# Kernel optimization log

Measured on AMD Instinct MI355X. Metric: run time of the kernel, lower is better.

Reference implementation:

```python
import jax, jax.numpy as jnp
import numpy as np
import math

EMBED_DIM = 1024
NUM_HEADS = 16
HEAD_DIM = EMBED_DIM // NUM_HEADS
SEGMENT_LENGTHS = [2048, 4096]
DILATION_RATES = [1, 2]
B, N = 1, 8192
IS_CAUSAL = True


def setup_inputs() -> dict:
    key = jax.random.key(0)
    ks = jax.random.split(key, 12)
    def w(k):
        return (jax.random.normal(k, (EMBED_DIM, EMBED_DIM), dtype=jnp.float32) * 0.02)
    inp = {
        'query': jax.random.normal(ks[0], (B, N, EMBED_DIM), dtype=jnp.float32),
        'key':   jax.random.normal(ks[1], (B, N, EMBED_DIM), dtype=jnp.float32),
        'value': jax.random.normal(ks[2], (B, N, EMBED_DIM), dtype=jnp.float32),
        'Wq': w(ks[3]), 'bq': jnp.zeros((EMBED_DIM,), jnp.float32),
        'Wk': w(ks[4]), 'bk': jnp.zeros((EMBED_DIM,), jnp.float32),
        'Wv': w(ks[5]), 'bv': jnp.zeros((EMBED_DIM,), jnp.float32),
        'Wo': w(ks[6]), 'bo': jnp.zeros((EMBED_DIM,), jnp.float32),
    }
    return inp


def _dilated_group_attention(q, k, v, seg_len, dilation, offset, causal):
    # q,k,v: [B, N, Hg, D] -> dilated block attention within segments
    b, n, hg, d = q.shape
    nseg = n // seg_len
    m = seg_len // dilation  # dilated subsequence length per segment
    idx = offset + dilation * jnp.arange(m)  # positions inside a segment
    def gather(x):
        return x.reshape(b, nseg, seg_len, hg, d)[:, :, idx]  # [B,nseg,m,Hg,D]
    qs, ks_, vs = gather(q), gather(k), gather(v)
    scale = 1.0 / math.sqrt(d)
    # [B,nseg,Hg,m,m]
    scores = jnp.einsum('bnihd,bnjhd->bnhij', qs, ks_) * scale
    if causal:
        mask = jnp.tril(jnp.ones((m, m), dtype=bool))
        scores = jnp.where(mask, scores, jnp.finfo(scores.dtype).min)
    attn = jax.nn.softmax(scores, axis=-1)
    out = jnp.einsum('bnhij,bnjhd->bnihd', attn, vs)  # [B,nseg,m,Hg,D]
    # scatter dilated outputs back to full segment positions (others zero)
    full = jnp.zeros((b, nseg, seg_len, hg, d), dtype=out.dtype)
    full = full.at[:, :, idx].set(out)
    return full.reshape(b, n, hg, d)


def reference(query, key, value, Wq, bq, Wk, bk, Wv, bv, Wo, bo):
    b, n, e = query.shape
    q = query @ Wq.T + bq
    k = key @ Wk.T + bk
    v = value @ Wv.T + bv
    q = q.reshape(b, n, NUM_HEADS, HEAD_DIM)
    k = k.reshape(b, n, NUM_HEADS, HEAD_DIM)
    v = v.reshape(b, n, NUM_HEADS, HEAD_DIM)
    num_groups = len(SEGMENT_LENGTHS)
    hpg = NUM_HEADS // num_groups  # heads per (segment, dilation) group
    outs = []
    for g in range(num_groups):
        s, r = SEGMENT_LENGTHS[g], DILATION_RATES[g]
        off = g % r
        hsl = slice(g * hpg, (g + 1) * hpg)
        outs.append(_dilated_group_attention(q[:, :, hsl], k[:, :, hsl], v[:, :, hsl],
                                             s, r, off, IS_CAUSAL))
    attn_out = jnp.concatenate(outs, axis=2).reshape(b, n, e)
    return attn_out @ Wo.T + bo
```

## Files before the change

kernel.cpp:

```cpp
#include <hip/hip_runtime.h>
#include <hip/hip_bf16.h>

typedef __attribute__((ext_vector_type(8))) __bf16 bf16x8;
typedef __attribute__((ext_vector_type(8))) unsigned short us8;
typedef __attribute__((ext_vector_type(4))) float f32x4;
typedef __attribute__((ext_vector_type(16))) float f32x16;
typedef __attribute__((ext_vector_type(2))) unsigned int uint2v;

#define N_TOK 8192
#define EMB 1024

static __device__ __forceinline__ unsigned short f2bf(float f) {
  union { __bf16 b; unsigned short u; } c;
  c.b = (__bf16)f;
  return c.u;
}

static __device__ __forceinline__ f32x4 mfma16(bf16x8 a, bf16x8 b, f32x4 c) {
  return __builtin_amdgcn_mfma_f32_16x16x32_bf16(a, b, c, 0, 0, 0);
}
static __device__ __forceinline__ f32x16 mfma32(bf16x8 a, bf16x8 b, f32x16 c) {
  return __builtin_amdgcn_mfma_f32_32x32x16_bf16(a, b, c, 0, 0, 0);
}
static __device__ __forceinline__ unsigned int cvtpk(float lo, float hi) {
  unsigned int r;
  asm("v_cvt_pk_bf16_f32 %0, %1, %2" : "=v"(r) : "v"(lo), "v"(hi));
  return r;
}
static __device__ __forceinline__ void gload16(const unsigned short* g, unsigned short* l) {
  __builtin_amdgcn_global_load_lds(
      (const __attribute__((address_space(1))) unsigned int*)g,
      (__attribute__((address_space(3))) unsigned int*)l, 16, 0, 0);
}

__global__ __launch_bounds__(256) void convall(
    const float* __restrict__ X0, const float* __restrict__ X1, const float* __restrict__ X2,
    const float* __restrict__ W0, const float* __restrict__ W1,
    const float* __restrict__ W2, const float* __restrict__ W3,
    unsigned short* __restrict__ Dq, unsigned short* __restrict__ Dk,
    unsigned short* __restrict__ Dv, unsigned short* __restrict__ Wb)
{
  const int bid = blockIdx.x;
  const float* src;
  unsigned short* dst;
  long base;
  if (bid < 6144) {
    const int t = bid >> 11;
    const int b = bid & 2047;
    src = (t == 0) ? X0 : (t == 1) ? X1 : X2;
    dst = (t == 0) ? Dq : (t == 1) ? Dk : Dv;
    base = ((long)b * 256 + threadIdx.x) * 16;
  } else {
    const int r = bid - 6144;
    const int t = r >> 8;
    const int b = r & 255;
    src = (t == 0) ? W0 : (t == 1) ? W1 : (t == 2) ? W2 : W3;
    dst = Wb + (size_t)t * EMB * EMB;
    base = ((long)b * 256 + threadIdx.x) * 16;
  }
  float4 f0 = *(const float4*)(src + base);
  float4 f1 = *(const float4*)(src + base + 4);
  float4 f2 = *(const float4*)(src + base + 8);
  float4 f3 = *(const float4*)(src + base + 12);
  us8 p0, p1;
  p0[0]=f2bf(f0.x); p0[1]=f2bf(f0.y); p0[2]=f2bf(f0.z); p0[3]=f2bf(f0.w);
  p0[4]=f2bf(f1.x); p0[5]=f2bf(f1.y); p0[6]=f2bf(f1.z); p0[7]=f2bf(f1.w);
  p1[0]=f2bf(f2.x); p1[1]=f2bf(f2.y); p1[2]=f2bf(f2.z); p1[3]=f2bf(f2.w);
  p1[4]=f2bf(f3.x); p1[5]=f2bf(f3.y); p1[6]=f2bf(f3.z); p1[7]=f2bf(f3.w);
  *(us8*)(dst + base)     = p0;
  *(us8*)(dst + base + 8) = p1;
}

__global__ __launch_bounds__(256) void qkv_gemm4(
    const unsigned short* __restrict__ Xq, const unsigned short* __restrict__ Xk,
    const unsigned short* __restrict__ Xv, const unsigned short* __restrict__ Wb,
    const float* __restrict__ bq, const float* __restrict__ bk, const float* __restrict__ bv,
    unsigned short* __restrict__ O0, unsigned short* __restrict__ O1, unsigned short* __restrict__ O2)
{
  __shared__ __align__(16) unsigned short As[128 * 32];
  __shared__ __align__(16) unsigned short Bs[128 * 32];

  const int z = blockIdx.z;
  const unsigned short* X = (z == 0) ? Xq : (z == 1) ? Xk : Xv;
  const unsigned short* W = Wb + (size_t)z * EMB * EMB;
  const float* bias = (z == 0) ? bq : (z == 1) ? bk : bv;

  const int lin  = blockIdx.x;
  const int work = (lin & 7) * 64 + (lin >> 3);
  const long brow = (long)(work >> 3) * 128;
  const long bcol = (long)(work & 7) * 128;

  const int tid  = threadIdx.x;
  const int lane = tid & 63;
  const int w    = tid >> 6;
  const int wrb  = (w >> 1) * 64;
  const int wcb  = (w & 1) * 64;
  const int r16  = lane & 15;
  const int kq   = (lane >> 4) * 8;
  const int rq   = (lane >> 4) * 4;

  const int srow = lane >> 2;
  const int scol = (lane & 3) * 8;
  const unsigned short* Ag0 = X + (brow + w*32      + srow) * (long)EMB + scol;
  const unsigned short* Ag1 = X + (brow + w*32 + 16 + srow) * (long)EMB + scol;
  const unsigned short* Bg0 = W + (bcol + w*32      + srow) * (long)EMB + scol;
  const unsigned short* Bg1 = W + (bcol + w*32 + 16 + srow) * (long)EMB + scol;
  unsigned short* Al0 = As + w * 1024;
  unsigned short* Al1 = As + w * 1024 + 512;
  unsigned short* Bl0 = Bs + w * 1024;
  unsigned short* Bl1 = Bs + w * 1024 + 512;

  const f32x4 zz = {0.f, 0.f, 0.f, 0.f};
  f32x4 acc[4][4];
#pragma unroll
  for (int i = 0; i < 4; ++i)
#pragma unroll
    for (int j = 0; j < 4; ++j) acc[i][j] = zz;

  for (int k0 = 0; k0 < EMB; k0 += 32) {
    __syncthreads();
    gload16(Ag0 + k0, Al0);
    gload16(Ag1 + k0, Al1);
    gload16(Bg0 + k0, Bl0);
    gload16(Bg1 + k0, Bl1);
    __syncthreads();

    bf16x8 av[4], bv_[4];
#pragma unroll
    for (int mi = 0; mi < 4; ++mi) av[mi]  = *(const bf16x8*)&As[(wrb + mi*16 + r16)*32 + kq];
#pragma unroll
    for (int ni = 0; ni < 4; ++ni) bv_[ni] = *(const bf16x8*)&Bs[(wcb + ni*16 + r16)*32 + kq];
#pragma unroll
    for (int mi = 0; mi < 4; ++mi)
#pragma unroll
      for (int ni = 0; ni < 4; ++ni)
        acc[mi][ni] = mfma16(av[mi], bv_[ni], acc[mi][ni]);
  }

#pragma unroll
  for (int ni = 0; ni < 4; ++ni) {
    const long col = bcol + wcb + ni*16 + r16;
    const float bval = bias[col];
#pragma unroll
    for (int mi = 0; mi < 4; ++mi)
#pragma unroll
      for (int jr = 0; jr < 4; ++jr) {
        const long row = brow + wrb + mi*16 + rq + jr;
        const float v = acc[mi][ni][jr] + bval;
        if (z == 2) {
          long r = row;
          if (col >= 512) {
            const long seg = row >> 12;
            const long pp = row & 4095;
            r = (seg << 12) + ((pp & 1) ? (pp >> 1) : 2048 + (pp >> 1));
          }
          O2[col * (long)N_TOK + r] = f2bf(v);
        } else {
          unsigned short* O = (z == 0) ? O0 : O1;
          O[row * (long)EMB + col] = f2bf(v);
        }
      }
  }
}

__global__ __launch_bounds__(128) void attn_dilated7(
    const unsigned short* __restrict__ Qp, const unsigned short* __restrict__ Kp,
    const unsigned short* __restrict__ Vt, unsigned short* __restrict__ AO)
{
  __shared__ __align__(16) unsigned short Ks[2][64][72];
  __shared__ __align__(16) unsigned short Vs[2][64][72];

  const int z   = blockIdx.z;
  const int g1  = (z >= 4);
  const int dil = g1 ? 2 : 1;
  const int off = g1 ? 1 : 0;
  const long segb = g1 ? (long)(z - 4) * 4096 : (long)z * 2048;
  const int h   = (g1 ? 8 : 0) + blockIdx.y;
  const int h64 = h * 64;

  const int bx   = (int)blockIdx.x;
  const int tid  = threadIdx.x;
  const int lane = tid & 63;
  const int w    = tid >> 6;
  const int q5   = lane & 31;
  const int hh   = lane >> 5;

  const int srow = tid >> 1;
  const int sc   = (tid & 1) * 32;

  const float SC2 = 0.18033688011112042f;

#pragma unroll
  for (int ph = 0; ph < 2; ++ph) {
    const int hf = ph ? bx : 31 - bx;
    const int qq = hf*64 + w*32 + q5;
    const long qrow = segb + off + (long)dil * qq;

    bf16x8 qf[4];
    {
      const unsigned short* qsrc = Qp + qrow * EMB + h64 + 8*hh;
#pragma unroll
      for (int s = 0; s < 4; ++s) qf[s] = *(const bf16x8*)(qsrc + 16*s);
    }

    float l_run = 0.f;
    f32x16 o0, o1;
#pragma unroll
    for (int r = 0; r < 16; ++r) { o0[r] = 0.f; o1[r] = 0.f; }

    us8 kr0, kr1, kr2, kr3, vr0, vr1, vr2, vr3;
    {
      const long gk = segb + off + (long)dil * srow;
      const unsigned short* ksrc = Kp + gk*EMB + h64 + sc;
      kr0 = *(const us8*)ksrc;        kr1 = *(const us8*)(ksrc + 8);
      kr2 = *(const us8*)(ksrc + 16); kr3 = *(const us8*)(ksrc + 24);
      const unsigned short* vsrc = Vt + (long)(h64 + srow)*N_TOK + segb + sc;
      vr0 = *(const us8*)vsrc;        vr1 = *(const us8*)(vsrc + 8);
      vr2 = *(const us8*)(vsrc + 16); vr3 = *(const us8*)(vsrc + 24);
      *(us8*)&Ks[0][srow][sc]    = kr0; *(us8*)&Ks[0][srow][sc+8]  = kr1;
      *(us8*)&Ks[0][srow][sc+16] = kr2; *(us8*)&Ks[0][srow][sc+24] = kr3;
      *(us8*)&Vs[0][srow][sc]    = vr0; *(us8*)&Vs[0][srow][sc+8]  = vr1;
      *(us8*)&Vs[0][srow][sc+16] = vr2; *(us8*)&Vs[0][srow][sc+24] = vr3;
    }
    __syncthreads();
    int cur = 0;

    for (int j = 0; j <= hf; ++j) {
      if (j < hf) {
        const long gk = segb + off + (long)dil * ((j+1)*64 + srow);
        const unsigned short* ksrc = Kp + gk*EMB + h64 + sc;
        kr0 = *(const us8*)ksrc;        kr1 = *(const us8*)(ksrc + 8);
        kr2 = *(const us8*)(ksrc + 16); kr3 = *(const us8*)(ksrc + 24);
        const unsigned short* vsrc = Vt + (long)(h64 + srow)*N_TOK + segb + (j+1)*64 + sc;
        vr0 = *(const us8*)vsrc;        vr1 = *(const us8*)(vsrc + 8);
        vr2 = *(const us8*)(vsrc + 16); vr3 = *(const us8*)(vsrc + 24);
      }

      f32x16 sa0, sa1;
#pragma unroll
      for (int r = 0; r < 16; ++r) { sa0[r] = 0.f; sa1[r] = 0.f; }
      __builtin_amdgcn_s_setprio(1);
#pragma unroll
      for (int s = 0; s < 4; ++s) {
        bf16x8 ka = *(const bf16x8*)&Ks[cur][q5][16*s + 8*hh];
        sa0 = mfma32(ka, qf[s], sa0);
      }
#pragma unroll
      for (int s = 0; s < 4; ++s) {
        bf16x8 kb = *(const bf16x8*)&Ks[cur][32 + q5][16*s + 8*hh];
        sa1 = mfma32(kb, qf[s], sa1);
      }
      __builtin_amdgcn_s_setprio(0);

      const bool diag   = (j == hf);
      const bool do_kb1 = (j < hf) || (w == 1);

      float sv[32];
#pragma unroll
      for (int r = 0; r < 16; ++r) {
        const int kof = (r&3) + 8*(r>>2);
        float v = fmaf(sa0[r], SC2, -8.0f);
        if (diag && (j*64 + kof + 4*hh > qq)) v = -1e30f;
        sv[r] = v;
      }
      if (do_kb1) {
#pragma unroll
        for (int r = 0; r < 16; ++r) {
          const int kof = (r&3) + 8*(r>>2);
          float v = fmaf(sa1[r], SC2, -8.0f);
          if (diag && (j*64 + 32 + kof + 4*hh > qq)) v = -1e30f;
          sv[16+r] = v;
        }
      }

      float psum = 0.f;
#pragma unroll
      for (int i = 0; i < 16; ++i) { float e = exp2f(sv[i]); sv[i] = e; psum += e; }
      if (do_kb1) {
#pragma unroll
        for (int i = 16; i < 32; ++i) { float e = exp2f(sv[i]); sv[i] = e; psum += e; }
      }
      {
        union { float f; unsigned int u; } pc; pc.f = psum;
        uint2v ps = __builtin_amdgcn_permlane32_swap(pc.u, pc.u, false, false);
        union { unsigned int u; float f; } a0, a1;
        a0.u = ps[0]; a1.u = ps[1];
        psum = a0.f + a1.f;
      }
      l_run += psum;

#pragma unroll
      for (int ks = 0; ks < 4; ++ks) {
        if (ks >= 2 && !do_kb1) continue;
        const unsigned int pk0 = cvtpk(sv[8*ks+0], sv[8*ks+1]);
        const unsigned int pk1 = cvtpk(sv[8*ks+2], sv[8*ks+3]);
        const unsigned int pk2 = cvtpk(sv[8*ks+4], sv[8*ks+5]);
        const unsigned int pk3 = cvtpk(sv[8*ks+6], sv[8*ks+7]);
        uint2v s02 = __builtin_amdgcn_permlane32_swap(pk0, pk2, false, false);
        uint2v s13 = __builtin_amdgcn_permlane32_swap(pk1, pk3, false, false);
        union { unsigned int wd[4]; bf16x8 v; } pu;
        pu.wd[0] = s02[0];
        pu.wd[1] = s13[0];
        pu.wd[2] = s02[1];
        pu.wd[3] = s13[1];
        __builtin_amdgcn_s_setprio(1);
        bf16x8 va = *(const bf16x8*)&Vs[cur][q5][16*ks + 8*hh];
        o0 = mfma32(va, pu.v, o0);
        bf16x8 vb = *(const bf16x8*)&Vs[cur][32 + q5][16*ks + 8*hh];
        o1 = mfma32(vb, pu.v, o1);
        __builtin_amdgcn_s_setprio(0);
      }

      if (j < hf) {
        *(us8*)&Ks[cur^1][srow][sc]    = kr0; *(us8*)&Ks[cur^1][srow][sc+8]  = kr1;
        *(us8*)&Ks[cur^1][srow][sc+16] = kr2; *(us8*)&Ks[cur^1][srow][sc+24] = kr3;
        *(us8*)&Vs[cur^1][srow][sc]    = vr0; *(us8*)&Vs[cur^1][srow][sc+8]  = vr1;
        *(us8*)&Vs[cur^1][srow][sc+16] = vr2; *(us8*)&Vs[cur^1][srow][sc+24] = vr3;
      }
      __syncthreads();
      cur ^= 1;
    }

    {
      const float inv = 1.f / l_run;
      unsigned short* dst = AO + qrow * EMB + h64;
#pragma unroll
      for (int r = 0; r < 16; ++r) {
        const int d = (r&3) + 8*(r>>2) + 4*hh;
        dst[d]      = f2bf(o0[r] * inv);
        dst[32 + d] = f2bf(o1[r] * inv);
      }
    }
  }
}

__global__ __launch_bounds__(256) void gemm_out4(
    const unsigned short* __restrict__ A, const unsigned short* __restrict__ Wb,
    const float* __restrict__ bias, float* __restrict__ outp)
{
  __shared__ __align__(16) unsigned short As[128 * 32];
  __shared__ __align__(16) unsigned short Bs[128 * 32];

  const int lin  = blockIdx.x;
  const int work = (lin & 7) * 64 + (lin >> 3);
  const long brow = (long)(work >> 3) * 128;
  const long bcol = (long)(work & 7) * 128;

  const int tid  = threadIdx.x;
  const int lane = tid & 63;
  const int w    = tid >> 6;
  const int wrb  = (w >> 1) * 64;
  const int wcb  = (w & 1) * 64;
  const int r16  = lane & 15;
  const int kq   = (lane >> 4) * 8;
  const int rq   = (lane >> 4) * 4;

  const int srow = lane >> 2;
  const int scol = (lane & 3) * 8;
  const unsigned short* Ag0 = A  + (brow + w*32      + srow) * (long)EMB + scol;
  const unsigned short* Ag1 = A  + (brow + w*32 + 16 + srow) * (long)EMB + scol;
  const unsigned short* Bg0 = Wb + (bcol + w*32      + srow) * (long)EMB + scol;
  const unsigned short* Bg1 = Wb + (bcol + w*32 + 16 + srow) * (long)EMB + scol;
  unsigned short* Al0 = As + w * 1024;
  unsigned short* Al1 = As + w * 1024 + 512;
  unsigned short* Bl0 = Bs + w * 1024;
  unsigned short* Bl1 = Bs + w * 1024 + 512;

  const f32x4 zz = {0.f, 0.f, 0.f, 0.f};
  f32x4 acc[4][4];
#pragma unroll
  for (int i = 0; i < 4; ++i)
#pragma unroll
    for (int j = 0; j < 4; ++j) acc[i][j] = zz;

  for (int k0 = 0; k0 < EMB; k0 += 32) {
    __syncthreads();
    gload16(Ag0 + k0, Al0);
    gload16(Ag1 + k0, Al1);
    gload16(Bg0 + k0, Bl0);
    gload16(Bg1 + k0, Bl1);
    __syncthreads();

    bf16x8 av[4], bv_[4];
#pragma unroll
    for (int mi = 0; mi < 4; ++mi) av[mi]  = *(const bf16x8*)&As[(wrb + mi*16 + r16)*32 + kq];
#pragma unroll
    for (int ni = 0; ni < 4; ++ni) bv_[ni] = *(const bf16x8*)&Bs[(wcb + ni*16 + r16)*32 + kq];
#pragma unroll
    for (int mi = 0; mi < 4; ++mi)
#pragma unroll
      for (int ni = 0; ni < 4; ++ni)
        acc[mi][ni] = mfma16(av[mi], bv_[ni], acc[mi][ni]);
  }

#pragma unroll
  for (int ni = 0; ni < 4; ++ni) {
    const long col = bcol + wcb + ni*16 + r16;
    const float bval = bias[col];
#pragma unroll
    for (int mi = 0; mi < 4; ++mi)
#pragma unroll
      for (int jr = 0; jr < 4; ++jr) {
        const long row = brow + wrb + mi*16 + rq + jr;
        outp[row * (long)EMB + col] = acc[mi][ni][jr] + bval;
      }
  }
}

extern "C" void kernel_launch(void* const* d_in, const int* in_sizes, int n_in,
                              void* d_out, int out_size, void* d_ws, size_t ws_size,
                              hipStream_t stream) {
  const float* query = (const float*)d_in[0];
  const float* key_  = (const float*)d_in[1];
  const float* value = (const float*)d_in[2];
  const float* Wq = (const float*)d_in[3];
  const float* bq = (const float*)d_in[4];
  const float* Wk = (const float*)d_in[5];
  const float* bk = (const float*)d_in[6];
  const float* Wv = (const float*)d_in[7];
  const float* bv = (const float*)d_in[8];
  const float* Wo = (const float*)d_in[9];
  const float* bo = (const float*)d_in[10];

  unsigned short* Qp  = (unsigned short*)d_ws;
  unsigned short* Kp  = Qp + (size_t)N_TOK * EMB;
  unsigned short* Vt  = Kp + (size_t)N_TOK * EMB;
  unsigned short* Wb  = Vt + (size_t)N_TOK * EMB;
  unsigned short* S   = Wb + (size_t)4 * EMB * EMB;
  unsigned short* Xbq = (unsigned short*)d_out;
  unsigned short* Xbk = Xbq + (size_t)N_TOK * EMB;
  unsigned short* Xbv = S;
  unsigned short* AO  = S;
  unsigned short* Wob = Wb + (size_t)3 * EMB * EMB;

  dim3 blk(256);

  hipLaunchKernelGGL(convall, dim3(7168), blk, 0, stream,
                     query, key_, value, Wq, Wk, Wv, Wo, Xbq, Xbk, Xbv, Wb);

  hipLaunchKernelGGL(qkv_gemm4, dim3(512, 1, 3), blk, 0, stream,
                     Xbq, Xbk, Xbv, Wb, bq, bk, bv, Qp, Kp, Vt);

  hipMemsetAsync(AO, 0, (size_t)N_TOK * EMB * 2, stream);

  hipLaunchKernelGGL(attn_dilated7, dim3(16, 8, 6), dim3(128), 0, stream, Qp, Kp, Vt, AO);

  hipLaunchKernelGGL(gemm_out4, dim3(512), blk, 0, stream, AO, Wob, bo, (float*)d_out);
}
```

Measured before the change: 229.2 us.

## Double-buffer LDS tiles in QKV and output GEMMs with async prefetch

Both projection GEMMs now keep two LDS buffers and prefetch the K-tile two steps ahead with direct global-to-LDS loads. Partial vmcnt waits and raw s_barrier replace the two __syncthreads per iteration. The aim is to overlap global load latency with MFMA work instead of stalling on every k-step. LDS use per block doubles, and the hand-placed waitcnt and barrier ordering has to be exactly right to avoid races.

New measurement: 233.7 us. About the same (+2.0%).

```diff
diff --git a/kernel.cpp b/kernel.cpp
--- a/kernel.cpp
+++ b/kernel.cpp
@@ -71,14 +71,14 @@
   *(us8*)(dst + base + 8) = p1;
 }
 
-__global__ __launch_bounds__(256) void qkv_gemm4(
+__global__ __launch_bounds__(256) void qkv_gemm6(
     const unsigned short* __restrict__ Xq, const unsigned short* __restrict__ Xk,
     const unsigned short* __restrict__ Xv, const unsigned short* __restrict__ Wb,
     const float* __restrict__ bq, const float* __restrict__ bk, const float* __restrict__ bv,
     unsigned short* __restrict__ O0, unsigned short* __restrict__ O1, unsigned short* __restrict__ O2)
 {
-  __shared__ __align__(16) unsigned short As[128 * 32];
-  __shared__ __align__(16) unsigned short Bs[128 * 32];
+  __shared__ __align__(16) unsigned short As[2][128 * 32];
+  __shared__ __align__(16) unsigned short Bs[2][128 * 32];
 
   const int z = blockIdx.z;
   const unsigned short* X = (z == 0) ? Xq : (z == 1) ? Xk : Xv;
@@ -105,10 +105,6 @@
   const unsigned short* Ag1 = X + (brow + w*32 + 16 + srow) * (long)EMB + scol;
   const unsigned short* Bg0 = W + (bcol + w*32      + srow) * (long)EMB + scol;
   const unsigned short* Bg1 = W + (bcol + w*32 + 16 + srow) * (long)EMB + scol;
-  unsigned short* Al0 = As + w * 1024;
-  unsigned short* Al1 = As + w * 1024 + 512;
-  unsigned short* Bl0 = Bs + w * 1024;
-  unsigned short* Bl1 = Bs + w * 1024 + 512;
 
   const f32x4 zz = {0.f, 0.f, 0.f, 0.f};
   f32x4 acc[4][4];
@@ -117,24 +113,47 @@
 #pragma unroll
     for (int j = 0; j < 4; ++j) acc[i][j] = zz;
 
-  for (int k0 = 0; k0 < EMB; k0 += 32) {
-    __syncthreads();
-    gload16(Ag0 + k0, Al0);
-    gload16(Ag1 + k0, Al1);
-    gload16(Bg0 + k0, Bl0);
-    gload16(Bg1 + k0, Bl1);
-    __syncthreads();
-
+  {
+    unsigned short* Al = &As[0][w * 1024];
+    unsigned short* Bl = &Bs[0][w * 1024];
+    gload16(Ag0, Al);      gload16(Ag1, Al + 512);
+    gload16(Bg0, Bl);      gload16(Bg1, Bl + 512);
+    Al = &As[1][w * 1024]; Bl = &Bs[1][w * 1024];
+    gload16(Ag0 + 32, Al); gload16(Ag1 + 32, Al + 512);
+    gload16(Bg0 + 32, Bl); gload16(Bg1 + 32, Bl + 512);
+  }
+  asm volatile("s_waitcnt vmcnt(4)" ::: "memory");
+  __builtin_amdgcn_sched_barrier(0);
+  __builtin_amdgcn_s_barrier();
+
+  for (int t = 0; t < 32; ++t) {
+    const int p = t & 1;
     bf16x8 av[4], bv_[4];
 #pragma unroll
-    for (int mi = 0; mi < 4; ++mi) av[mi]  = *(const bf16x8*)&As[(wrb + mi*16 + r16)*32 + kq];
-#pragma unroll
-    for (int ni = 0; ni < 4; ++ni) bv_[ni] = *(const bf16x8*)&Bs[(wcb + ni*16 + r16)*32 + kq];
+    for (int mi = 0; mi < 4; ++mi) av[mi]  = *(const bf16x8*)&As[p][(wrb + mi*16 + r16)*32 + kq];
+#pragma unroll
+    for (int ni = 0; ni < 4; ++ni) bv_[ni] = *(const bf16x8*)&Bs[p][(wcb + ni*16 + r16)*32 + kq];
 #pragma unroll
     for (int mi = 0; mi < 4; ++mi)
 #pragma unroll
       for (int ni = 0; ni < 4; ++ni)
         acc[mi][ni] = mfma16(av[mi], bv_[ni], acc[mi][ni]);
+
+    __builtin_amdgcn_s_barrier();
+    if (t < 30) {
+      const int kn = (t + 2) * 32;
+      unsigned short* Al = &As[p][w * 1024];
+      unsigned short* Bl = &Bs[p][w * 1024];
+      gload16(Ag0 + kn, Al);      gload16(Ag1 + kn, Al + 512);
+      gload16(Bg0 + kn, Bl);      gload16(Bg1 + kn, Bl + 512);
+      asm volatile("s_waitcnt vmcnt(4)" ::: "memory");
+      __builtin_amdgcn_sched_barrier(0);
+      __builtin_amdgcn_s_barrier();
+    } else if (t == 30) {
+      asm volatile("s_waitcnt vmcnt(0)" ::: "memory");
+      __builtin_amdgcn_sched_barrier(0);
+      __builtin_amdgcn_s_barrier();
+    }
   }
 
 #pragma unroll
@@ -334,12 +353,12 @@
   }
 }
 
-__global__ __launch_bounds__(256) void gemm_out4(
+__global__ __launch_bounds__(256) void gemm_out6(
     const unsigned short* __restrict__ A, const unsigned short* __restrict__ Wb,
     const float* __restrict__ bias, float* __restrict__ outp)
 {
-  __shared__ __align__(16) unsigned short As[128 * 32];
-  __shared__ __align__(16) unsigned short Bs[128 * 32];
+  __shared__ __align__(16) unsigned short As[2][128 * 32];
+  __shared__ __align__(16) unsigned short Bs[2][128 * 32];
 
   const int lin  = blockIdx.x;
   const int work = (lin & 7) * 64 + (lin >> 3);
@@ -361,10 +380,6 @@
   const unsigned short* Ag1 = A  + (brow + w*32 + 16 + srow) * (long)EMB + scol;
   const unsigned short* Bg0 = Wb + (bcol + w*32      + srow) * (long)EMB + scol;
   const unsigned short* Bg1 = Wb + (bcol + w*32 + 16 + srow) * (long)EMB + scol;
-  unsigned short* Al0 = As + w * 1024;
-  unsigned short* Al1 = As + w * 1024 + 512;
-  unsigned short* Bl0 = Bs + w * 1024;
-  unsigned short* Bl1 = Bs + w * 1024 + 512;
 
   const f32x4 zz = {0.f, 0.f, 0.f, 0.f};
   f32x4 acc[4][4];
@@ -373,24 +388,47 @@
 #pragma unroll
     for (int j = 0; j < 4; ++j) acc[i][j] = zz;
 
-  for (int k0 = 0; k0 < EMB; k0 += 32) {
-    __syncthreads();
-    gload16(Ag0 + k0, Al0);
-    gload16(Ag1 + k0, Al1);
-    gload16(Bg0 + k0, Bl0);
-    gload16(Bg1 + k0, Bl1);
-    __syncthreads();
-
+  {
+    unsigned short* Al = &As[0][w * 1024];
+    unsigned short* Bl = &Bs[0][w * 1024];
+    gload16(Ag0, Al);      gload16(Ag1, Al + 512);
+    gload16(Bg0, Bl);      gload16(Bg1, Bl + 512);
+    Al = &As[1][w * 1024]; Bl = &Bs[1][w * 1024];
+    gload16(Ag0 + 32, Al); gload16(Ag1 + 32, Al + 512);
+    gload16(Bg0 + 32, Bl); gload16(Bg1 + 32, Bl + 512);
+  }
+  asm volatile("s_waitcnt vmcnt(4)" ::: "memory");
+  __builtin_amdgcn_sched_barrier(0);
+  __builtin_amdgcn_s_barrier();
+
+  for (int t = 0; t < 32; ++t) {
+    const int p = t & 1;
     bf16x8 av[4], bv_[4];
 #pragma unroll
-    for (int mi = 0; mi < 4; ++mi) av[mi]  = *(const bf16x8*)&As[(wrb + mi*16 + r16)*32 + kq];
-#pragma unroll
-    for (int ni = 0; ni < 4; ++ni) bv_[ni] = *(const bf16x8*)&Bs[(wcb + ni*16 + r16)*32 + kq];
+    for (int mi = 0; mi < 4; ++mi) av[mi]  = *(const bf16x8*)&As[p][(wrb + mi*16 + r16)*32 + kq];
+#pragma unroll
+    for (int ni = 0; ni < 4; ++ni) bv_[ni] = *(const bf16x8*)&Bs[p][(wcb + ni*16 + r16)*32 + kq];
 #pragma unroll
     for (int mi = 0; mi < 4; ++mi)
 #pragma unroll
       for (int ni = 0; ni < 4; ++ni)
         acc[mi][ni] = mfma16(av[mi], bv_[ni], acc[mi][ni]);
+
+    __builtin_amdgcn_s_barrier();
+    if (t < 30) {
+      const int kn = (t + 2) * 32;
+      unsigned short* Al = &As[p][w * 1024];
+      unsigned short* Bl = &Bs[p][w * 1024];
+      gload16(Ag0 + kn, Al);      gload16(Ag1 + kn, Al + 512);
+      gload16(Bg0 + kn, Bl);      gload16(Bg1 + kn, Bl + 512);
+      asm volatile("s_waitcnt vmcnt(4)" ::: "memory");
+      __builtin_amdgcn_sched_barrier(0);
+      __builtin_amdgcn_s_barrier();
+    } else if (t == 30) {
+      asm volatile("s_waitcnt vmcnt(0)" ::: "memory");
+      __builtin_amdgcn_sched_barrier(0);
+      __builtin_amdgcn_s_barrier();
+    }
   }
 
 #pragma unroll
@@ -438,12 +476,12 @@
   hipLaunchKernelGGL(convall, dim3(7168), blk, 0, stream,
                      query, key_, value, Wq, Wk, Wv, Wo, Xbq, Xbk, Xbv, Wb);
 
-  hipLaunchKernelGGL(qkv_gemm4, dim3(512, 1, 3), blk, 0, stream,
+  hipLaunchKernelGGL(qkv_gemm6, dim3(512, 1, 3), blk, 0, stream,
                      Xbq, Xbk, Xbv, Wb, bq, bk, bv, Qp, Kp, Vt);
 
   hipMemsetAsync(AO, 0, (size_t)N_TOK * EMB * 2, stream);
 
   hipLaunchKernelGGL(attn_dilated7, dim3(16, 8, 6), dim3(128), 0, stream, Qp, Kp, Vt, AO);
 
-  hipLaunchKernelGGL(gemm_out4, dim3(512), blk, 0, stream, AO, Wob, bo, (float*)d_out);
-}
+  hipLaunchKernelGGL(gemm_out6, dim3(512), blk, 0, stream, AO, Wob, bo, (float*)d_out);
+}
```
